# Kernel tuning notes

Measured on AMD Instinct MI355X. Metric: run time of the kernel, lower is better.

The kernel has to match this reference:

```python
import jax, jax.numpy as jnp
import numpy as np
import math

H = 512
NH = 8
HD = H // NH


def _lin_params(key, out_dim, in_dim):
    k1, k2 = jax.random.split(key)
    bound = 1.0 / math.sqrt(in_dim)
    w = jax.random.uniform(k1, (out_dim, in_dim), minval=-bound, maxval=bound, dtype=jnp.float32)
    b = jax.random.uniform(k2, (out_dim,), minval=-bound, maxval=bound, dtype=jnp.float32)
    return w, b


def setup_inputs() -> dict:
    key = jax.random.key(0)
    ks = jax.random.split(key, 16)
    B, L = 8, 1024
    inp = {
        'hidden_states': jax.random.normal(ks[0], (B, L, H), dtype=jnp.float32),
        'text': jax.random.normal(ks[1], (B, L, H), dtype=jnp.float32),
    }
    names = ['q_img', 'k_img', 'v_img', 'q_txt', 'k_txt', 'v_txt', 'out_img', 'out_txt']
    for i, n in enumerate(names):
        w, b = _lin_params(ks[2 + i], H, H)
        inp['w_' + n] = w
        inp['b_' + n] = b
    wcat, bcat = _lin_params(ks[10], H, 2 * H)
    inp['w_cat'] = wcat
    inp['b_cat'] = bcat
    # nn.MultiheadAttention params: in_proj [3H, H], out_proj [H, H]
    inp['in_proj_w'] = jax.random.normal(ks[11], (3 * H, H), dtype=jnp.float32) * (1.0 / math.sqrt(H))
    inp['in_proj_b'] = jnp.zeros((3 * H,), dtype=jnp.float32)
    pw, pb = _lin_params(ks[12], H, H)
    inp['out_proj_w'] = pw
    inp['out_proj_b'] = pb
    return inp


def _lin(x, w, b):
    return x @ w.T + b


def _heads(x):
    B, L, _ = x.shape
    return x.reshape(B, L, NH, HD).transpose(0, 2, 1, 3)  # [B, NH, L, HD]


def _attn(q, k, v):
    # q,k,v: [B, NH, L, HD]; dropout is identity in eval mode
    scores = jnp.einsum('bhqd,bhkd->bhqk', q, k) / math.sqrt(HD)
    probs = jax.nn.softmax(scores, axis=-1)
    ctx = jnp.einsum('bhqk,bhkd->bhqd', probs, v)
    B, _, L, _ = ctx.shape
    return ctx.transpose(0, 2, 1, 3).reshape(B, L, H)


def reference(hidden_states, text,
              w_q_img, b_q_img, w_k_img, b_k_img, w_v_img, b_v_img,
              w_q_txt, b_q_txt, w_k_txt, b_k_txt, w_v_txt, b_v_txt,
              w_out_img, b_out_img, w_out_txt, b_out_txt,
              w_cat, b_cat, in_proj_w, in_proj_b, out_proj_w, out_proj_b):
    q_img = _heads(_lin(hidden_states, w_q_img, b_q_img))
    k_img = _heads(_lin(hidden_states, w_k_img, b_k_img))
    v_img = _heads(_lin(hidden_states, w_v_img, b_v_img))
    q_txt = _heads(_lin(text, w_q_txt, b_q_txt))
    k_txt = _heads(_lin(text, w_k_txt, b_k_txt))
    v_txt = _heads(_lin(text, w_v_txt, b_v_txt))

    ctx_img = _attn(q_img, k_img, v_img)
    ctx_txt = _attn(q_txt, k_txt, v_txt)
    ctx_it = _attn(q_img, k_txt, v_txt)
    ctx_ti = _attn(q_txt, k_img, v_img)

    out_img = _lin((ctx_img + ctx_it) * 0.5, w_out_img, b_out_img)
    out_txt = _lin((ctx_txt + ctx_ti) * 0.5, w_out_txt, b_out_txt)
    out = _lin(jnp.concatenate([out_img, out_txt], axis=2), w_cat, b_cat)

    # attention pooling (nn.MultiheadAttention self-attention, batch-major math)
    qkv = _lin(out, in_proj_w, in_proj_b)
    q, k, v = jnp.split(qkv, 3, axis=-1)
    ctx = _attn(_heads(q), _heads(k), _heads(v))
    return _lin(ctx, out_proj_w, out_proj_b)
```

## Files before the change

kernel.cpp:

```cpp
#include <hip/hip_runtime.h>

typedef unsigned short u16;
typedef __attribute__((ext_vector_type(4))) unsigned short u16x4;
typedef __attribute__((ext_vector_type(8))) unsigned short u16x8;
typedef __attribute__((ext_vector_type(4))) float f32x4;
typedef __attribute__((ext_vector_type(8))) __bf16 bf16x8;
typedef __attribute__((ext_vector_type(2))) unsigned int u32x2;
typedef __attribute__((ext_vector_type(4))) unsigned int u32x4;

#define WS_XH    0UL
#define WS_XT    8388608UL
#define WS_W     16777216UL
#define WS_BQI   24117248UL
#define WS_BQT   24123392UL
#define WS_QKVI  24129536UL
#define WS_QKVT  49295360UL
#define WS_VTI   74461184UL
#define WS_VTT   82849792UL
#define WS_CTXIA 91238400UL
#define WS_CTXTA 99627008UL
#define WS_OCAT  108015616UL
#define WS_OUT2  24129536UL
#define WS_QKVP  32518144UL
#define WS_VTP   57683968UL
#define WS_CTXP  66072576UL

#define SCALE_LOG2E_O8 0.18033688011112042f

__device__ __forceinline__ u16 f2bf(float f) {
  unsigned u = __float_as_uint(f);
  u += 0x7fffu + ((u >> 16) & 1u);
  return (u16)(u >> 16);
}
__device__ __forceinline__ float bf2f(u16 v) {
  return __uint_as_float(((unsigned)v) << 16);
}
__device__ __forceinline__ bf16x8 as_bf(u16x8 v) { return __builtin_bit_cast(bf16x8, v); }
__device__ __forceinline__ f32x4 mfma16(bf16x8 a, bf16x8 b, f32x4 c) {
  return __builtin_amdgcn_mfma_f32_16x16x32_bf16(a, b, c, 0, 0, 0);
}
__device__ __forceinline__ unsigned pack_bf2(float lo, float hi) {
  unsigned a = __float_as_uint(lo) + 0x8000u;
  unsigned b = __float_as_uint(hi) + 0x8000u;
  return __builtin_amdgcn_perm(b, a, 0x07060302);
}

__global__ __launch_bounds__(256) void cvt_f32_bf16(const float* __restrict__ s,
                                                    u16* __restrict__ d, int n) {
  int i = (blockIdx.x * 256 + threadIdx.x) * 4;
  if (i >= n) return;
  float4 v = *(const float4*)(s + i);
  u16x4 o;
  o[0] = f2bf(v.x); o[1] = f2bf(v.y); o[2] = f2bf(v.z); o[3] = f2bf(v.w);
  *(u16x4*)(d + i) = o;
}

__global__ __launch_bounds__(256) void prep_weights(
    const float* __restrict__ wqi, const float* __restrict__ wki, const float* __restrict__ wvi,
    const float* __restrict__ wqt, const float* __restrict__ wkt, const float* __restrict__ wvt,
    const float* __restrict__ woi, const float* __restrict__ wot,
    const float* __restrict__ wc,  const float* __restrict__ wip, const float* __restrict__ wop,
    const float* __restrict__ bqi, const float* __restrict__ bki, const float* __restrict__ bvi,
    const float* __restrict__ bqt, const float* __restrict__ bkt, const float* __restrict__ bvt,
    u16* __restrict__ wdst, float* __restrict__ bi, float* __restrict__ bt) {
  int i = blockIdx.x * 256 + threadIdx.x;
  if (i < 786432) {
    const float* s = i < 262144 ? wqi : (i < 524288 ? wki : wvi);
    wdst[i] = f2bf(s[i & 262143]);
  } else if (i < 1572864) {
    int j = i - 786432;
    const float* s = j < 262144 ? wqt : (j < 524288 ? wkt : wvt);
    wdst[i] = f2bf(s[j & 262143]);
  } else if (i < 1835008) wdst[i] = f2bf(woi[i - 1572864]);
  else if (i < 2097152)   wdst[i] = f2bf(wot[i - 1835008]);
  else if (i < 2621440)   wdst[i] = f2bf(wc [i - 2097152]);
  else if (i < 3407872)   wdst[i] = f2bf(wip[i - 2621440]);
  else if (i < 3670016)   wdst[i] = f2bf(wop[i - 3407872]);
  else if (i < 3671552) {
    int j = i - 3670016;
    bi[j] = j < 512 ? bqi[j] : (j < 1024 ? bki[j - 512] : bvi[j - 1024]);
  } else if (i < 3673088) {
    int j = i - 3671552;
    bt[j] = j < 512 ? bqt[j] : (j < 1024 ? bkt[j - 512] : bvt[j - 1024]);
  }
}

__global__ __launch_bounds__(256) void gemm_bf16(
    const u16* __restrict__ A, const u16* __restrict__ A2, int lda,
    const u16* __restrict__ W,
    const float* __restrict__ bias, u16* __restrict__ C, int ldc, int coff, int K,
    int f32out, int qcols, float qscale, u16* __restrict__ vtout) {
  __shared__ __align__(16) u16 As[2][8 * 512];
  __shared__ __align__(16) u16 Bs[2][8 * 512];
  const int tid = threadIdx.x, lane = tid & 63, wv = tid >> 6;
  const int wm = wv >> 1, wn = wv & 1;
  const int ln15 = lane & 15;
  const int m0 = blockIdx.x * 128, n0 = blockIdx.y * 128;

  const int srow = lane & 15, skc = lane >> 4;
  const u16* gA0 = A + (long)(m0 + wv * 32 + srow) * lda + skc * 8;
  const u16* gA1 = gA0 + (long)16 * lda;
  const u16* gW0 = W + (long)(n0 + wv * 32 + srow) * K + skc * 8;
  const u16* gW1 = gW0 + (long)16 * K;
  const u16* gA20 = A2 + (long)(m0 + wv * 32 + srow) * lda + skc * 8;
  const u16* gA21 = gA20 + (long)16 * lda;

  f32x4 acc[4][4];
#pragma unroll
  for (int j = 0; j < 4; ++j) {
    float bv = bias[n0 + wn * 64 + j * 16 + ln15];
#pragma unroll
    for (int i = 0; i < 4; ++i) acc[i][j] = f32x4{bv, bv, bv, bv};
  }

  u16x8 ra0 = *(const u16x8*)(gA0);
  u16x8 ra1 = *(const u16x8*)(gA1);
  u16x8 rb0 = *(const u16x8*)(gW0);
  u16x8 rb1 = *(const u16x8*)(gW1);
  u16x8 rc0, rc1;
  if (A2) { rc0 = *(const u16x8*)(gA20); rc1 = *(const u16x8*)(gA21); }

  int buf = 0;
  for (int k0 = 0; k0 < K; k0 += 32, buf ^= 1) {
    u16x8 wa0 = ra0, wa1 = ra1;
    if (A2) {
#pragma unroll
      for (int u = 0; u < 8; ++u) {
        wa0[u] = f2bf(bf2f(ra0[u]) + bf2f(rc0[u]));
        wa1[u] = f2bf(bf2f(ra1[u]) + bf2f(rc1[u]));
      }
    }
    u16* la = As[buf] + (wv * 2) * 512;
    u16* lb = Bs[buf] + (wv * 2) * 512;
    *(u16x8*)(la + lane * 8) = wa0;
    *(u16x8*)(la + 512 + lane * 8) = wa1;
    *(u16x8*)(lb + lane * 8) = rb0;
    *(u16x8*)(lb + 512 + lane * 8) = rb1;
    if (k0 + 32 < K) {
      ra0 = *(const u16x8*)(gA0 + k0 + 32);
      ra1 = *(const u16x8*)(gA1 + k0 + 32);
      rb0 = *(const u16x8*)(gW0 + k0 + 32);
      rb1 = *(const u16x8*)(gW1 + k0 + 32);
      if (A2) { rc0 = *(const u16x8*)(gA20 + k0 + 32); rc1 = *(const u16x8*)(gA21 + k0 + 32); }
    }
    __syncthreads();

    bf16x8 af[4], bfr[4];
#pragma unroll
    for (int i = 0; i < 4; ++i)
      af[i] = as_bf(*(const u16x8*)(As[buf] + (wm * 4 + i) * 512 + lane * 8));
#pragma unroll
    for (int j = 0; j < 4; ++j)
      bfr[j] = as_bf(*(const u16x8*)(Bs[buf] + (wn * 4 + j) * 512 + lane * 8));
#pragma unroll
    for (int i = 0; i < 4; ++i)
#pragma unroll
      for (int j = 0; j < 4; ++j) acc[i][j] = mfma16(af[i], bfr[j], acc[i][j]);
  }
  const int quad = lane >> 4;
  const int qr4 = quad * 4;
  if (vtout && n0 >= 1024) {
#pragma unroll
    for (int j = 0; j < 4; ++j) {
      int col = n0 + wn * 64 + j * 16 + ln15;
      int dg = col - 1024;
      long vtrow = ((long)0 * 8 + (dg >> 6)) * 64 + (dg & 63);
#pragma unroll
      for (int i = 0; i < 4; ++i) {
        int row0 = m0 + wm * 64 + i * 16 + qr4;
        long vr = ((long)(row0 >> 10) * 8 + (dg >> 6)) * 64 + (dg & 63);
        u16x4 ov;
#pragma unroll
        for (int r = 0; r < 4; ++r) ov[r] = f2bf(acc[i][j][r]);
        *(u16x4*)(vtout + vr * 1024 + (row0 & 1023)) = ov;
      }
      (void)vtrow;
    }
    return;
  }
  float colsc[4];
#pragma unroll
  for (int j = 0; j < 4; ++j)
    colsc[j] = (n0 + wn * 64 + j * 16 < qcols) ? qscale : 1.0f;
#pragma unroll
  for (int i = 0; i < 4; ++i)
#pragma unroll
    for (int r = 0; r < 4; ++r) {
      int row = m0 + wm * 64 + i * 16 + qr4 + r;
      long cidx = (long)row * ldc + coff + n0 + wn * 64 + ln15;
      if (f32out) {
        float* cf = (float*)C + cidx;
#pragma unroll
        for (int j = 0; j < 4; ++j) cf[j * 16] = acc[i][j][r] * colsc[j];
      } else {
        u16* cp = C + cidx;
#pragma unroll
        for (int j = 0; j < 4; ++j) cp[j * 16] = f2bf(acc[i][j][r] * colsc[j]);
      }
    }
}

template <int NQF>
__global__ __launch_bounds__(256) void attn_flash(
    const u16* __restrict__ Q, int ldq,
    const u16* __restrict__ KA, const u16* __restrict__ VTA,
    const u16* __restrict__ KB, const u16* __restrict__ VTB, int ldk,
    u16* __restrict__ OA, u16* __restrict__ OB, int ldo, float outscale) {
  __shared__ __align__(16) u16 Kt[32][72];
  __shared__ __align__(16) u16 Vt[64][40];
  const int tid = threadIdx.x, lane = tid & 63, wv = tid >> 6;
  const int ln15 = lane & 15, quad = lane >> 4, q8 = quad * 8;
  const int h = blockIdx.y, b = blockIdx.z;

  const u16 *K, *VT;
  u16* O;
  int qtile;
  if (KB != nullptr) {
    qtile = blockIdx.x >> 1;
    int phase = blockIdx.x & 1;
    K = phase ? KB : KA;
    VT = phase ? VTB : VTA;
    O = phase ? OB : OA;
  } else {
    qtile = blockIdx.x;
    K = KA; VT = VTA; O = OA;
  }
  const long qrow = (long)b * 1024 + qtile * (NQF * 64) + wv * (NQF * 16);

  bf16x8 qf[NQF][2];
#pragma unroll
  for (int qi = 0; qi < NQF; ++qi) {
    const u16* qp = Q + (qrow + qi * 16 + ln15) * ldq + h * 64;
    qf[qi][0] = as_bf(*(const u16x8*)(qp + q8));
    qf[qi][1] = as_bf(*(const u16x8*)(qp + 32 + q8));
  }

  u16x8 ones_u;
#pragma unroll
  for (int j = 0; j < 8; ++j) ones_u[j] = 0x3F80;
  const bf16x8 onesb = as_bf(ones_u);

  const int kk = tid >> 3, dc = (tid & 7) * 8;
  const int vd = tid >> 2;
  const int ko = (tid & 3) * 8;
  const int vs0 = ((tid & 1) << 4) | ((tid & 2) << 1);
  const u16* Kbase = K + ((long)b * 1024 + kk) * ldk + h * 64 + dc;
  const u16* Vbase = VT + ((long)((b * 8 + h) * 64 + vd)) * 1024 + ko;

  f32x4 o[NQF][4];
  f32x4 lacc[NQF];
#pragma unroll
  for (int qi = 0; qi < NQF; ++qi) {
    lacc[qi] = f32x4{0.f, 0.f, 0.f, 0.f};
#pragma unroll
    for (int j = 0; j < 4; ++j) o[qi][j] = f32x4{0.f, 0.f, 0.f, 0.f};
  }

  u32x4 kreg = *(const u32x4*)(Kbase);
  u32x4 vreg = *(const u32x4*)(Vbase);

  for (int k0 = 0; k0 < 1024; k0 += 32) {
    *(u32x4*)(&Kt[kk][dc]) = kreg;
    u32x2 vlo = {vreg[0], vreg[1]}, vhi = {vreg[2], vreg[3]};
    *(u32x2*)(&Vt[vd][vs0]) = vlo;
    *(u32x2*)(&Vt[vd][vs0 + 8]) = vhi;
    __syncthreads();
    if (k0 + 32 < 1024) {
      kreg = *(const u32x4*)(Kbase + (long)(k0 + 32) * ldk);
      vreg = *(const u32x4*)(Vbase + (k0 + 32));
    }

    f32x4 st[2][NQF];
#pragma unroll
    for (int kt = 0; kt < 2; ++kt) {
      bf16x8 ka0 = as_bf(*(const u16x8*)(&Kt[kt * 16 + ln15][q8]));
      bf16x8 ka1 = as_bf(*(const u16x8*)(&Kt[kt * 16 + ln15][32 + q8]));
#pragma unroll
      for (int qi = 0; qi < NQF; ++qi) {
        f32x4 z = f32x4{0.f, 0.f, 0.f, 0.f};
        z = mfma16(ka0, qf[qi][0], z);
        z = mfma16(ka1, qf[qi][1], z);
        st[kt][qi] = z;
      }
    }

    bf16x8 pb[NQF];
#pragma unroll
    for (int qi = 0; qi < NQF; ++qi) {
      float p00 = __builtin_amdgcn_exp2f(st[0][qi][0]);
      float p01 = __builtin_amdgcn_exp2f(st[0][qi][1]);
      float p02 = __builtin_amdgcn_exp2f(st[0][qi][2]);
      float p03 = __builtin_amdgcn_exp2f(st[0][qi][3]);
      float p10 = __builtin_amdgcn_exp2f(st[1][qi][0]);
      float p11 = __builtin_amdgcn_exp2f(st[1][qi][1]);
      float p12 = __builtin_amdgcn_exp2f(st[1][qi][2]);
      float p13 = __builtin_amdgcn_exp2f(st[1][qi][3]);
      u32x4 pk;
      pk[0] = pack_bf2(p00, p01);
      pk[1] = pack_bf2(p02, p03);
      pk[2] = pack_bf2(p10, p11);
      pk[3] = pack_bf2(p12, p13);
      pb[qi] = as_bf(__builtin_bit_cast(u16x8, pk));
      lacc[qi] = mfma16(onesb, pb[qi], lacc[qi]);
    }
#pragma unroll
    for (int j = 0; j < 4; ++j) {
      bf16x8 av = as_bf(*(const u16x8*)(&Vt[j * 16 + ln15][q8]));
#pragma unroll
      for (int qi = 0; qi < NQF; ++qi) o[qi][j] = mfma16(av, pb[qi], o[qi][j]);
    }
    __syncthreads();
  }

#pragma unroll
  for (int qi = 0; qi < NQF; ++qi) {
    float inv = outscale / lacc[qi][0];
    long row = qrow + qi * 16 + ln15;
#pragma unroll
    for (int j = 0; j < 4; ++j) {
      u16x4 ov;
#pragma unroll
      for (int r = 0; r < 4; ++r) ov[r] = f2bf(o[qi][j][r] * inv);
      *(u16x4*)(O + row * ldo + h * 64 + j * 16 + quad * 4) = ov;
    }
  }
}

extern "C" void kernel_launch(void* const* d_in, const int* in_sizes, int n_in,
                              void* d_out, int out_size, void* d_ws, size_t ws_size,
                              hipStream_t stream) {
  const float* hidden = (const float*)d_in[0];
  const float* text   = (const float*)d_in[1];
  const float* wqi = (const float*)d_in[2];  const float* bqi = (const float*)d_in[3];
  const float* wki = (const float*)d_in[4];  const float* bki = (const float*)d_in[5];
  const float* wvi = (const float*)d_in[6];  const float* bvi = (const float*)d_in[7];
  const float* wqt = (const float*)d_in[8];  const float* bqt = (const float*)d_in[9];
  const float* wkt = (const float*)d_in[10]; const float* bkt = (const float*)d_in[11];
  const float* wvt = (const float*)d_in[12]; const float* bvt = (const float*)d_in[13];
  const float* woi = (const float*)d_in[14]; const float* boi = (const float*)d_in[15];
  const float* wot = (const float*)d_in[16]; const float* bot = (const float*)d_in[17];
  const float* wc  = (const float*)d_in[18]; const float* bc  = (const float*)d_in[19];
  const float* wip = (const float*)d_in[20]; const float* bip = (const float*)d_in[21];
  const float* wop = (const float*)d_in[22]; const float* bop = (const float*)d_in[23];

  char* ws = (char*)d_ws;
  u16* XH    = (u16*)(ws + WS_XH);
  u16* XT    = (u16*)(ws + WS_XT);
  u16* WB    = (u16*)(ws + WS_W);
  float* BQI = (float*)(ws + WS_BQI);
  float* BQT = (float*)(ws + WS_BQT);
  u16* QKVI  = (u16*)(ws + WS_QKVI);
  u16* QKVT  = (u16*)(ws + WS_QKVT);
  u16* VTI   = (u16*)(ws + WS_VTI);
  u16* VTT   = (u16*)(ws + WS_VTT);
  u16* CTXIA = (u16*)(ws + WS_CTXIA);
  u16* CTXIB = (u16*)(ws + WS_XH);
  u16* CTXTA = (u16*)(ws + WS_CTXTA);
  u16* CTXTB = (u16*)(ws + WS_XT);
  u16* OCAT  = (u16*)(ws + WS_OCAT);
  u16* OUT2  = (u16*)(ws + WS_OUT2);
  u16* QKVP  = (u16*)(ws + WS_QKVP);
  u16* VTP   = (u16*)(ws + WS_VTP);
  u16* CTXP  = (u16*)(ws + WS_CTXP);

  u16* WQKVI = WB;
  u16* WQKVT = WB + 786432;
  u16* WOUTI = WB + 1572864;
  u16* WOUTT = WB + 1835008;
  u16* WCAT  = WB + 2097152;
  u16* WINP  = WB + 2621440;
  u16* WOUTP = WB + 3407872;

  const int NACT = 8192 * 512;

  cvt_f32_bf16<<<dim3(NACT / 1024), 256, 0, stream>>>(hidden, XH, NACT);
  cvt_f32_bf16<<<dim3(NACT / 1024), 256, 0, stream>>>(text, XT, NACT);
  prep_weights<<<dim3(14348), 256, 0, stream>>>(wqi, wki, wvi, wqt, wkt, wvt, woi, wot,
                                                wc, wip, wop, bqi, bki, bvi, bqt, bkt, bvt,
                                                WB, BQI, BQT);
  gemm_bf16<<<dim3(64, 12), 256, 0, stream>>>(XH, nullptr, 512, WQKVI, BQI, QKVI, 1536, 0, 512,
                                              0, 512, SCALE_LOG2E_O8, VTI);
  gemm_bf16<<<dim3(64, 12), 256, 0, stream>>>(XT, nullptr, 512, WQKVT, BQT, QKVT, 1536, 0, 512,
                                              0, 512, SCALE_LOG2E_O8, VTT);
  attn_flash<2><<<dim3(16, 8, 8), 256, 0, stream>>>(QKVI, 1536, QKVI + 512, VTI,
                                                    QKVT + 512, VTT, 1536,
                                                    CTXIA, CTXIB, 512, 0.5f);
  attn_flash<2><<<dim3(16, 8, 8), 256, 0, stream>>>(QKVT, 1536, QKVT + 512, VTT,
                                                    QKVI + 512, VTI, 1536,
                                                    CTXTA, CTXTB, 512, 0.5f);
  gemm_bf16<<<dim3(64, 4), 256, 0, stream>>>(CTXIA, CTXIB, 512, WOUTI, boi, OCAT, 1024, 0, 512,
                                             0, 0, 1.0f, nullptr);
  gemm_bf16<<<dim3(64, 4), 256, 0, stream>>>(CTXTA, CTXTB, 512, WOUTT, bot, OCAT, 1024, 512, 512,
                                             0, 0, 1.0f, nullptr);
  gemm_bf16<<<dim3(64, 4), 256, 0, stream>>>(OCAT, nullptr, 1024, WCAT, bc, OUT2, 512, 0, 1024,
                                             0, 0, 1.0f, nullptr);
  gemm_bf16<<<dim3(64, 12), 256, 0, stream>>>(OUT2, nullptr, 512, WINP, bip, QKVP, 1536, 0, 512,
                                              0, 512, SCALE_LOG2E_O8, VTP);
  attn_flash<1><<<dim3(16, 8, 8), 256, 0, stream>>>(QKVP, 1536, QKVP + 512, VTP,
                                                    nullptr, nullptr, 1536,
                                                    CTXP, nullptr, 512, 1.0f);
  gemm_bf16<<<dim3(64, 4), 256, 0, stream>>>(CTXP, nullptr, 512, WOUTP, bop, (u16*)d_out, 512,
                                             0, 512, 1, 0, 1.0f, nullptr);
}
```

Before: 402.3 us.

## Batch paired launches via grid z and double-buffer attention LDS tiles

Merges the paired conversion, QKV projection, attention and output-projection launches into single launches, selecting operands by blockIdx.z through pointer offsets. This cuts launch count and gives each launch a larger grid to fill the GPU. The attention kernel double-buffers its K/V LDS tiles so one barrier per iteration can be dropped, uses the hardware packed bf16 convert instead of manual rounding, and sets an occupancy hint. In the GEMM, the barrier moves ahead of the next global prefetch. The shifted barrier may change how load latency overlaps with compute, and the occupancy hint may cause register spills.

```diff
diff --git a/kernel.cpp b/kernel.cpp
--- a/kernel.cpp
+++ b/kernel.cpp
@@ -39,14 +39,18 @@
 __device__ __forceinline__ f32x4 mfma16(bf16x8 a, bf16x8 b, f32x4 c) {
   return __builtin_amdgcn_mfma_f32_16x16x32_bf16(a, b, c, 0, 0, 0);
 }
-__device__ __forceinline__ unsigned pack_bf2(float lo, float hi) {
-  unsigned a = __float_as_uint(lo) + 0x8000u;
-  unsigned b = __float_as_uint(hi) + 0x8000u;
-  return __builtin_amdgcn_perm(b, a, 0x07060302);
-}
-
-__global__ __launch_bounds__(256) void cvt_f32_bf16(const float* __restrict__ s,
-                                                    u16* __restrict__ d, int n) {
+__device__ __forceinline__ unsigned cvt_pk_bf16(float lo, float hi) {
+  unsigned r;
+  asm("v_cvt_pk_bf16_f32 %0, %1, %2" : "=v"(r) : "v"(lo), "v"(hi));
+  return r;
+}
+
+__global__ __launch_bounds__(256) void cvt_f32_bf16(const float* __restrict__ s0,
+                                                    const float* __restrict__ s1,
+                                                    u16* __restrict__ d0,
+                                                    u16* __restrict__ d1, int n) {
+  const float* s = blockIdx.y ? s1 : s0;
+  u16* d = blockIdx.y ? d1 : d0;
   int i = (blockIdx.x * 256 + threadIdx.x) * 4;
   if (i >= n) return;
   float4 v = *(const float4*)(s + i);
@@ -89,7 +93,15 @@
     const u16* __restrict__ A, const u16* __restrict__ A2, int lda,
     const u16* __restrict__ W,
     const float* __restrict__ bias, u16* __restrict__ C, int ldc, int coff, int K,
-    int f32out, int qcols, float qscale, u16* __restrict__ vtout) {
+    int f32out, int qcols, float qscale, u16* __restrict__ vtout,
+    long zdA, long zdA2, long zdW, long zdB, long zdC, long zdVT, int zdCoff) {
+  if (blockIdx.z) {
+    A += zdA;
+    if (A2) A2 += zdA2;
+    W += zdW; bias += zdB; C += zdC;
+    if (vtout) vtout += zdVT;
+    coff += zdCoff;
+  }
   __shared__ __align__(16) u16 As[2][8 * 512];
   __shared__ __align__(16) u16 Bs[2][8 * 512];
   const int tid = threadIdx.x, lane = tid & 63, wv = tid >> 6;
@@ -136,6 +148,7 @@
     *(u16x8*)(la + 512 + lane * 8) = wa1;
     *(u16x8*)(lb + lane * 8) = rb0;
     *(u16x8*)(lb + 512 + lane * 8) = rb1;
+    __syncthreads();
     if (k0 + 32 < K) {
       ra0 = *(const u16x8*)(gA0 + k0 + 32);
       ra1 = *(const u16x8*)(gA1 + k0 + 32);
@@ -143,7 +156,6 @@
       rb1 = *(const u16x8*)(gW1 + k0 + 32);
       if (A2) { rc0 = *(const u16x8*)(gA20 + k0 + 32); rc1 = *(const u16x8*)(gA21 + k0 + 32); }
     }
-    __syncthreads();
 
     bf16x8 af[4], bfr[4];
 #pragma unroll
@@ -164,7 +176,6 @@
     for (int j = 0; j < 4; ++j) {
       int col = n0 + wn * 64 + j * 16 + ln15;
       int dg = col - 1024;
-      long vtrow = ((long)0 * 8 + (dg >> 6)) * 64 + (dg & 63);
 #pragma unroll
       for (int i = 0; i < 4; ++i) {
         int row0 = m0 + wm * 64 + i * 16 + qr4;
@@ -174,7 +185,6 @@
         for (int r = 0; r < 4; ++r) ov[r] = f2bf(acc[i][j][r]);
         *(u16x4*)(vtout + vr * 1024 + (row0 & 1023)) = ov;
       }
-      (void)vtrow;
     }
     return;
   }
@@ -200,30 +210,36 @@
     }
 }
 
-template <int NQF>
-__global__ __launch_bounds__(256) void attn_flash(
-    const u16* __restrict__ Q, int ldq,
-    const u16* __restrict__ KA, const u16* __restrict__ VTA,
-    const u16* __restrict__ KB, const u16* __restrict__ VTB, int ldk,
-    u16* __restrict__ OA, u16* __restrict__ OB, int ldo, float outscale) {
-  __shared__ __align__(16) u16 Kt[32][72];
-  __shared__ __align__(16) u16 Vt[64][40];
+template <int NQF, bool DUAL>
+__global__ __launch_bounds__(256, 8) void attn_flash(
+    const u16* __restrict__ Q0, const u16* __restrict__ Q1, int ldq,
+    const u16* __restrict__ K0, const u16* __restrict__ VT0,
+    const u16* __restrict__ K1, const u16* __restrict__ VT1, int ldk,
+    u16* __restrict__ O00, u16* __restrict__ O01,
+    u16* __restrict__ O10, u16* __restrict__ O11, int ldo, float outscale) {
+  __shared__ __align__(16) u16 Kt[2][32][72];
+  __shared__ __align__(16) u16 Vt[2][64][40];
   const int tid = threadIdx.x, lane = tid & 63, wv = tid >> 6;
   const int ln15 = lane & 15, quad = lane >> 4, q8 = quad * 8;
-  const int h = blockIdx.y, b = blockIdx.z;
-
-  const u16 *K, *VT;
+  const int h = blockIdx.y;
+
+  const u16 *Q, *K, *VT;
   u16* O;
-  int qtile;
-  if (KB != nullptr) {
+  int qtile, b;
+  if constexpr (DUAL) {
     qtile = blockIdx.x >> 1;
-    int phase = blockIdx.x & 1;
-    K = phase ? KB : KA;
-    VT = phase ? VTB : VTA;
-    O = phase ? OB : OA;
+    const int phase = blockIdx.x & 1;
+    const int qsel = blockIdx.z & 1;
+    b = blockIdx.z >> 1;
+    Q = qsel ? Q1 : Q0;
+    const int ksel = qsel ^ phase;
+    K = ksel ? K1 : K0;
+    VT = ksel ? VT1 : VT0;
+    O = qsel ? (phase ? O11 : O10) : (phase ? O01 : O00);
   } else {
     qtile = blockIdx.x;
-    K = KA; VT = VTA; O = OA;
+    b = blockIdx.z;
+    Q = Q0; K = K0; VT = VT0; O = O00;
   }
   const long qrow = (long)b * 1024 + qtile * (NQF * 64) + wv * (NQF * 16);
 
@@ -259,11 +275,12 @@
   u32x4 kreg = *(const u32x4*)(Kbase);
   u32x4 vreg = *(const u32x4*)(Vbase);
 
-  for (int k0 = 0; k0 < 1024; k0 += 32) {
-    *(u32x4*)(&Kt[kk][dc]) = kreg;
+  int cur = 0;
+  for (int k0 = 0; k0 < 1024; k0 += 32, cur ^= 1) {
+    *(u32x4*)(&Kt[cur][kk][dc]) = kreg;
     u32x2 vlo = {vreg[0], vreg[1]}, vhi = {vreg[2], vreg[3]};
-    *(u32x2*)(&Vt[vd][vs0]) = vlo;
-    *(u32x2*)(&Vt[vd][vs0 + 8]) = vhi;
+    *(u32x2*)(&Vt[cur][vd][vs0]) = vlo;
+    *(u32x2*)(&Vt[cur][vd][vs0 + 8]) = vhi;
     __syncthreads();
     if (k0 + 32 < 1024) {
       kreg = *(const u32x4*)(Kbase + (long)(k0 + 32) * ldk);
@@ -273,8 +290,8 @@
     f32x4 st[2][NQF];
 #pragma unroll
     for (int kt = 0; kt < 2; ++kt) {
-      bf16x8 ka0 = as_bf(*(const u16x8*)(&Kt[kt * 16 + ln15][q8]));
-      bf16x8 ka1 = as_bf(*(const u16x8*)(&Kt[kt * 16 + ln15][32 + q8]));
+      bf16x8 ka0 = as_bf(*(const u16x8*)(&Kt[cur][kt * 16 + ln15][q8]));
+      bf16x8 ka1 = as_bf(*(const u16x8*)(&Kt[cur][kt * 16 + ln15][32 + q8]));
 #pragma unroll
       for (int qi = 0; qi < NQF; ++qi) {
         f32x4 z = f32x4{0.f, 0.f, 0.f, 0.f};
@@ -296,20 +313,19 @@
       float p12 = __builtin_amdgcn_exp2f(st[1][qi][2]);
       float p13 = __builtin_amdgcn_exp2f(st[1][qi][3]);
       u32x4 pk;
-      pk[0] = pack_bf2(p00, p01);
-      pk[1] = pack_bf2(p02, p03);
-      pk[2] = pack_bf2(p10, p11);
-      pk[3] = pack_bf2(p12, p13);
+      pk[0] = cvt_pk_bf16(p00, p01);
+      pk[1] = cvt_pk_bf16(p02, p03);
+      pk[2] = cvt_pk_bf16(p10, p11);
+      pk[3] = cvt_pk_bf16(p12, p13);
       pb[qi] = as_bf(__builtin_bit_cast(u16x8, pk));
       lacc[qi] = mfma16(onesb, pb[qi], lacc[qi]);
     }
 #pragma unroll
     for (int j = 0; j < 4; ++j) {
-      bf16x8 av = as_bf(*(const u16x8*)(&Vt[j * 16 + ln15][q8]));
+      bf16x8 av = as_bf(*(const u16x8*)(&Vt[cur][j * 16 + ln15][q8]));
 #pragma unroll
       for (int qi = 0; qi < NQF; ++qi) o[qi][j] = mfma16(av, pb[qi], o[qi][j]);
     }
-    __syncthreads();
   }
 
 #pragma unroll
@@ -364,41 +380,37 @@
   u16* CTXP  = (u16*)(ws + WS_CTXP);
 
   u16* WQKVI = WB;
-  u16* WQKVT = WB + 786432;
   u16* WOUTI = WB + 1572864;
-  u16* WOUTT = WB + 1835008;
   u16* WCAT  = WB + 2097152;
   u16* WINP  = WB + 2621440;
   u16* WOUTP = WB + 3407872;
 
   const int NACT = 8192 * 512;
 
-  cvt_f32_bf16<<<dim3(NACT / 1024), 256, 0, stream>>>(hidden, XH, NACT);
-  cvt_f32_bf16<<<dim3(NACT / 1024), 256, 0, stream>>>(text, XT, NACT);
+  cvt_f32_bf16<<<dim3(NACT / 1024, 2), 256, 0, stream>>>(hidden, text, XH, XT, NACT);
   prep_weights<<<dim3(14348), 256, 0, stream>>>(wqi, wki, wvi, wqt, wkt, wvt, woi, wot,
                                                 wc, wip, wop, bqi, bki, bvi, bqt, bkt, bvt,
                                                 WB, BQI, BQT);
-  gemm_bf16<<<dim3(64, 12), 256, 0, stream>>>(XH, nullptr, 512, WQKVI, BQI, QKVI, 1536, 0, 512,
-                                              0, 512, SCALE_LOG2E_O8, VTI);
-  gemm_bf16<<<dim3(64, 12), 256, 0, stream>>>(XT, nullptr, 512, WQKVT, BQT, QKVT, 1536, 0, 512,
-                                              0, 512, SCALE_LOG2E_O8, VTT);
-  attn_flash<2><<<dim3(16, 8, 8), 256, 0, stream>>>(QKVI, 1536, QKVI + 512, VTI,
-                                                    QKVT + 512, VTT, 1536,
-                                                    CTXIA, CTXIB, 512, 0.5f);
-  attn_flash<2><<<dim3(16, 8, 8), 256, 0, stream>>>(QKVT, 1536, QKVT + 512, VTT,
-                                                    QKVI + 512, VTI, 1536,
-                                                    CTXTA, CTXTB, 512, 0.5f);
-  gemm_bf16<<<dim3(64, 4), 256, 0, stream>>>(CTXIA, CTXIB, 512, WOUTI, boi, OCAT, 1024, 0, 512,
-                                             0, 0, 1.0f, nullptr);
-  gemm_bf16<<<dim3(64, 4), 256, 0, stream>>>(CTXTA, CTXTB, 512, WOUTT, bot, OCAT, 1024, 512, 512,
-                                             0, 0, 1.0f, nullptr);
-  gemm_bf16<<<dim3(64, 4), 256, 0, stream>>>(OCAT, nullptr, 1024, WCAT, bc, OUT2, 512, 0, 1024,
-                                             0, 0, 1.0f, nullptr);
-  gemm_bf16<<<dim3(64, 12), 256, 0, stream>>>(OUT2, nullptr, 512, WINP, bip, QKVP, 1536, 0, 512,
-                                              0, 512, SCALE_LOG2E_O8, VTP);
-  attn_flash<1><<<dim3(16, 8, 8), 256, 0, stream>>>(QKVP, 1536, QKVP + 512, VTP,
-                                                    nullptr, nullptr, 1536,
-                                                    CTXP, nullptr, 512, 1.0f);
-  gemm_bf16<<<dim3(64, 4), 256, 0, stream>>>(CTXP, nullptr, 512, WOUTP, bop, (u16*)d_out, 512,
-                                             0, 512, 1, 0, 1.0f, nullptr);
-}
+  gemm_bf16<<<dim3(64, 12, 2), 256, 0, stream>>>(
+      XH, nullptr, 512, WQKVI, BQI, QKVI, 1536, 0, 512, 0, 512, SCALE_LOG2E_O8, VTI,
+      4194304, 0, 786432, 1536, 12582912, 4194304, 0);
+  attn_flash<2, true><<<dim3(16, 8, 16), 256, 0, stream>>>(
+      QKVI, QKVT, 1536, QKVI + 512, VTI, QKVT + 512, VTT, 1536,
+      CTXIA, CTXIB, CTXTA, CTXTB, 512, 0.5f);
+  gemm_bf16<<<dim3(64, 4, 2), 256, 0, stream>>>(
+      CTXIA, CTXIB, 512, WOUTI, boi, OCAT, 1024, 0, 512, 0, 0, 1.0f, nullptr,
+      4194304, 4194304, 262144, (long)(bot - boi),
+      0, 0, 512);
+  gemm_bf16<<<dim3(64, 4, 1), 256, 0, stream>>>(
+      OCAT, nullptr, 1024, WCAT, bc, OUT2, 512, 0, 1024, 0, 0, 1.0f, nullptr,
+      0, 0, 0, 0, 0, 0, 0);
+  gemm_bf16<<<dim3(64, 12, 1), 256, 0, stream>>>(
+      OUT2, nullptr, 512, WINP, bip, QKVP, 1536, 0, 512, 0, 512, SCALE_LOG2E_O8, VTP,
+      0, 0, 0, 0, 0, 0, 0);
+  attn_flash<1, false><<<dim3(16, 8, 8), 256, 0, stream>>>(
+      QKVP, nullptr, 1536, QKVP + 512, VTP, nullptr, nullptr, 1536,
+      CTXP, nullptr, nullptr, nullptr, 512, 1.0f);
+  gemm_bf16<<<dim3(64, 4, 1), 256, 0, stream>>>(
+      CTXP, nullptr, 512, WOUTP, bop, (u16*)d_out, 512, 0, 512, 1, 0, 1.0f, nullptr,
+      0, 0, 0, 0, 0, 0, 0);
+}
```

Result: slower. 1.231 ms (+205.9%).
